# Optimization experiments

Measured on AMD Instinct MI355X. Metric: run time of the kernel, lower is better.

The kernel has to match this reference:

```python
import jax, jax.numpy as jnp
import numpy as np

N_NODES = 50000
N_EDGES = 500000
IN_FEATS = 96
OUT_FEATS = 128
N_ETYPES = 4
N_STEPS = 3  # feat is never updated (no GRU), so each step is identical


def setup_inputs() -> dict:
    key = jax.random.key(0)
    k1, k2, k3, k4, k5 = jax.random.split(key, 5)
    feat = jax.random.normal(k1, (N_NODES, IN_FEATS), dtype=jnp.float32)
    etypes = jax.random.randint(k2, (N_EDGES,), 0, N_ETYPES, dtype=jnp.int64)
    src = jax.random.randint(k3, (N_EDGES,), 0, N_NODES, dtype=jnp.int64)
    dst = jax.random.randint(k4, (N_EDGES,), 0, N_NODES, dtype=jnp.int64)
    # per-etype Linear(out_feats, out_feats): W[i] is [out, out], xavier-normal-ish
    gain = float(np.sqrt(2.0))  # calculate_gain('relu')
    std = gain * np.sqrt(2.0 / (OUT_FEATS + OUT_FEATS))
    W = jax.random.normal(k5, (N_ETYPES, OUT_FEATS, OUT_FEATS), dtype=jnp.float32) * std
    b = jnp.zeros((N_ETYPES, OUT_FEATS), dtype=jnp.float32)
    return {"feat": feat, "etypes": etypes, "src": src, "dst": dst, "W": W, "b": b}


def reference(feat, etypes, src, dst, W, b):
    n_nodes = feat.shape[0]
    # h_i^0 = [x_i || 0]  -> pad to out_feats
    h = jnp.pad(feat, ((0, 0), (0, OUT_FEATS - feat.shape[1])))  # [N, out]
    # Since there is no GRU, h never changes across n_steps; each step's 'a'
    # is identical, so one aggregation suffices (faithful to returned value).
    h_src = h[src]  # [E, out] gather
    msgs = jnp.zeros((h_src.shape[0], OUT_FEATS), dtype=h.dtype)
    for i in range(N_ETYPES):
        # Linear: x @ W_i^T + b_i, applied only to edges of type i
        m_i = h_src @ W[i].T + b[i]  # [E, out]
        msgs = jnp.where((etypes == i)[:, None], m_i, msgs)
    # scatter-sum messages to destination nodes
    a = jax.ops.segment_sum(msgs, dst, num_segments=n_nodes)  # [N, out]
    return a
```

## Files before the change

kernel.cpp:

```cpp
#include <hip/hip_runtime.h>
#include <hip/hip_bf16.h>

#define N_NODES 50000
#define N_EDGES 500000
#define IN_FEATS 96
#define OUT_FEATS 128
#define N_ETYPES 4
#define KCAT (N_ETYPES * IN_FEATS)

typedef __attribute__((ext_vector_type(8))) short short8;
typedef __attribute__((ext_vector_type(4))) float f32x4;

static __device__ inline short f2bf_bits(float f) {
    __hip_bfloat16 h = __float2bfloat16(f);
    return *reinterpret_cast<short*>(&h);
}
static __device__ inline unsigned pack2bf(float lo, float hi) {
    unsigned l = (unsigned short)f2bf_bits(lo);
    unsigned h = (unsigned short)f2bf_bits(hi);
    return l | (h << 16);
}

__global__ __launch_bounds__(256) void k_init(int* __restrict__ deg,
                                              const float* __restrict__ W,
                                              unsigned* __restrict__ Wb_u32) {
    int g = blockIdx.x * 256 + threadIdx.x;
    if (g < N_NODES) deg[g] = 0;
    if (g < 512 * 48) {
        int row = g / 48, pair = g % 48;
        float lo = W[(size_t)row * OUT_FEATS + pair * 2];
        float hi = W[(size_t)row * OUT_FEATS + pair * 2 + 1];
        Wb_u32[g] = pack2bf(lo, hi);
    }
}

__global__ __launch_bounds__(256) void k_hist(const int* __restrict__ dst,
                                              int* __restrict__ deg,
                                              int* __restrict__ rank) {
    int e = blockIdx.x * 256 + threadIdx.x;
    if (e < N_EDGES) rank[e] = atomicAdd(&deg[dst[e]], 1);
}

__global__ __launch_bounds__(256) void k_scan1(const int* __restrict__ in, int n,
                                               int* __restrict__ out, int* __restrict__ bsum) {
    int g = blockIdx.x * 256 + threadIdx.x;
    int lane = threadIdx.x & 63, wave = threadIdx.x >> 6;
    int v = (g < n) ? in[g] : 0;
    int orig = v;
    for (int off = 1; off < 64; off <<= 1) {
        int u = __shfl_up(v, off);
        if (lane >= off) v += u;
    }
    __shared__ int wsum[4];
    if (lane == 63) wsum[wave] = v;
    __syncthreads();
    if (threadIdx.x == 0) {
        int s = 0;
        for (int w = 0; w < 4; ++w) { int t = wsum[w]; wsum[w] = s; s += t; }
        bsum[blockIdx.x] = s;
    }
    __syncthreads();
    int excl = v - orig + wsum[wave];
    if (g < n) out[g] = excl;
}

__global__ __launch_bounds__(256) void k_scan3(int* __restrict__ pos, const int* __restrict__ bscan, int n) {
    int g = blockIdx.x * 256 + threadIdx.x;
    if (g < n) pos[g] += bscan[blockIdx.x];
}

__global__ __launch_bounds__(256) void k_bin(const int* __restrict__ dst, const int* __restrict__ src,
                                             const int* __restrict__ etypes,
                                             const int* __restrict__ pos, const int* __restrict__ rank,
                                             int* __restrict__ packed) {
    int e = blockIdx.x * 256 + threadIdx.x;
    if (e < N_EDGES) {
        int slot = pos[dst[e]] + rank[e];
        packed[slot] = src[e] | (etypes[e] << 16);
    }
}

__global__ __launch_bounds__(64) void k_agg(const float2* __restrict__ feat2,
                                            const int* __restrict__ pos, const int* __restrict__ deg,
                                            const int* __restrict__ packed,
                                            unsigned* __restrict__ Scat_u32,
                                            float* __restrict__ counts) {
    const int d = blockIdx.x;
    const int lane = threadIdx.x;
    const bool act = lane < 48;
    const int start = pos[d], cnt = deg[d];

    float2 a0 = {0.f, 0.f}, a1 = {0.f, 0.f}, a2 = {0.f, 0.f}, a3 = {0.f, 0.f};
    int c0 = 0, c1 = 0, c2 = 0, c3 = 0;
    const float2 zero = {0.f, 0.f};

    int i = 0;
    for (; i + 4 <= cnt; i += 4) {
        int p0 = packed[start + i + 0];
        int p1 = packed[start + i + 1];
        int p2 = packed[start + i + 2];
        int p3 = packed[start + i + 3];
        float2 v0 = act ? feat2[(size_t)(p0 & 0xFFFF) * 48 + lane] : zero;
        float2 v1 = act ? feat2[(size_t)(p1 & 0xFFFF) * 48 + lane] : zero;
        float2 v2 = act ? feat2[(size_t)(p2 & 0xFFFF) * 48 + lane] : zero;
        float2 v3 = act ? feat2[(size_t)(p3 & 0xFFFF) * 48 + lane] : zero;
        int e0 = p0 >> 16, e1 = p1 >> 16, e2 = p2 >> 16, e3 = p3 >> 16;
        if (e0 == 0) { a0.x += v0.x; a0.y += v0.y; ++c0; }
        else if (e0 == 1) { a1.x += v0.x; a1.y += v0.y; ++c1; }
        else if (e0 == 2) { a2.x += v0.x; a2.y += v0.y; ++c2; }
        else              { a3.x += v0.x; a3.y += v0.y; ++c3; }
        if (e1 == 0) { a0.x += v1.x; a0.y += v1.y; ++c0; }
        else if (e1 == 1) { a1.x += v1.x; a1.y += v1.y; ++c1; }
        else if (e1 == 2) { a2.x += v1.x; a2.y += v1.y; ++c2; }
        else              { a3.x += v1.x; a3.y += v1.y; ++c3; }
        if (e2 == 0) { a0.x += v2.x; a0.y += v2.y; ++c0; }
        else if (e2 == 1) { a1.x += v2.x; a1.y += v2.y; ++c1; }
        else if (e2 == 2) { a2.x += v2.x; a2.y += v2.y; ++c2; }
        else              { a3.x += v2.x; a3.y += v2.y; ++c3; }
        if (e3 == 0) { a0.x += v3.x; a0.y += v3.y; ++c0; }
        else if (e3 == 1) { a1.x += v3.x; a1.y += v3.y; ++c1; }
        else if (e3 == 2) { a2.x += v3.x; a2.y += v3.y; ++c2; }
        else              { a3.x += v3.x; a3.y += v3.y; ++c3; }
    }
    for (; i < cnt; ++i) {
        int p = packed[start + i];
        float2 v = act ? feat2[(size_t)(p & 0xFFFF) * 48 + lane] : zero;
        int e = p >> 16;
        if (e == 0) { a0.x += v.x; a0.y += v.y; ++c0; }
        else if (e == 1) { a1.x += v.x; a1.y += v.y; ++c1; }
        else if (e == 2) { a2.x += v.x; a2.y += v.y; ++c2; }
        else              { a3.x += v.x; a3.y += v.y; ++c3; }
    }

    if (act) {
        size_t base = (size_t)d * (KCAT / 2) + lane;
        Scat_u32[base]       = pack2bf(a0.x, a0.y);
        Scat_u32[base + 48]  = pack2bf(a1.x, a1.y);
        Scat_u32[base + 96]  = pack2bf(a2.x, a2.y);
        Scat_u32[base + 144] = pack2bf(a3.x, a3.y);
    }
    if (lane < 4) counts[d * 4 + lane] = (float)(lane == 0 ? c0 : lane == 1 ? c1 : lane == 2 ? c2 : c3);
}

#define LDT 104

__global__ __launch_bounds__(256) void k_gemm(const __hip_bfloat16* __restrict__ Scat,
                                              const short* __restrict__ Wb,
                                              const float* __restrict__ b,
                                              const float* __restrict__ counts,
                                              float* __restrict__ out) {
    __shared__ __align__(16) __hip_bfloat16 As[128][LDT];
    __shared__ __align__(16) __hip_bfloat16 Bs[128][LDT];
    const int m0 = blockIdx.x * 128;
    const int tid = threadIdx.x, lane = tid & 63, wave = tid >> 6;
    const int wm = wave >> 1, wn = wave & 1;

    f32x4 acc[4][4];
#pragma unroll
    for (int i = 0; i < 4; ++i)
#pragma unroll
        for (int jj = 0; jj < 4; ++jj) acc[i][jj] = (f32x4){0.f, 0.f, 0.f, 0.f};

    for (int ks = 0; ks < 4; ++ks) {
#pragma unroll
        for (int it = 0; it < 6; ++it) {
            int idx = tid + it * 256;
            int row = idx / 12, c8 = idx % 12;
            int gm = m0 + row;
            if (gm > N_NODES - 1) gm = N_NODES - 1;
            short8 v = *reinterpret_cast<const short8*>(&Scat[(size_t)gm * KCAT + ks * IN_FEATS + c8 * 8]);
            *reinterpret_cast<short8*>(&As[row][c8 * 8]) = v;
        }
#pragma unroll
        for (int it = 0; it < 6; ++it) {
            int idx = tid + it * 256;
            int row = idx / 12, c8 = idx % 12;
            short8 v = *reinterpret_cast<const short8*>(&Wb[((size_t)ks * OUT_FEATS + row) * IN_FEATS + c8 * 8]);
            *reinterpret_cast<short8*>(&Bs[row][c8 * 8]) = v;
        }
        __syncthreads();
#pragma unroll
        for (int kk = 0; kk < 3; ++kk) {
            short8 af[4], bf[4];
#pragma unroll
            for (int mi = 0; mi < 4; ++mi)
                af[mi] = *reinterpret_cast<const short8*>(&As[wm * 64 + mi * 16 + (lane & 15)][kk * 32 + (lane >> 4) * 8]);
#pragma unroll
            for (int ni = 0; ni < 4; ++ni)
                bf[ni] = *reinterpret_cast<const short8*>(&Bs[wn * 64 + ni * 16 + (lane & 15)][kk * 32 + (lane >> 4) * 8]);
#pragma unroll
            for (int mi = 0; mi < 4; ++mi)
#pragma unroll
                for (int ni = 0; ni < 4; ++ni)
                    acc[mi][ni] = __builtin_amdgcn_mfma_f32_16x16x32_bf16(af[mi], bf[ni], acc[mi][ni], 0, 0, 0);
        }
        __syncthreads();
    }

#pragma unroll
    for (int mi = 0; mi < 4; ++mi) {
#pragma unroll
        for (int r = 0; r < 4; ++r) {
            int m = m0 + wm * 64 + mi * 16 + (lane >> 4) * 4 + r;
            if (m < N_NODES) {
                float4 c4 = *reinterpret_cast<const float4*>(&counts[m * 4]);
#pragma unroll
                for (int ni = 0; ni < 4; ++ni) {
                    int n = wn * 64 + ni * 16 + (lane & 15);
                    float bias = c4.x * b[n] + c4.y * b[OUT_FEATS + n] +
                                 c4.z * b[2 * OUT_FEATS + n] + c4.w * b[3 * OUT_FEATS + n];
                    out[(size_t)m * OUT_FEATS + n] = acc[mi][ni][r] + bias;
                }
            }
        }
    }
}

__global__ __launch_bounds__(256) void edge_direct(const float* __restrict__ feat,
                                                   const int* __restrict__ etypes,
                                                   const int* __restrict__ src,
                                                   const int* __restrict__ dst,
                                                   const float* __restrict__ W,
                                                   const float* __restrict__ b,
                                                   float* __restrict__ out) {
    int gid = blockIdx.x * 256 + threadIdx.x;
    int e = gid >> 7;
    int j = gid & 127;
    if (e >= N_EDGES) return;
    int et = etypes[e];
    int s = src[e];
    int d = dst[e];
    const float* f = feat + (size_t)s * IN_FEATS;
    const float* w = W + ((size_t)et * OUT_FEATS + j) * OUT_FEATS;
    float acc = b[et * OUT_FEATS + j];
    for (int k = 0; k < IN_FEATS; ++k) acc += f[k] * w[k];
    atomicAdd(&out[(size_t)d * OUT_FEATS + j], acc);
}

extern "C" void kernel_launch(void* const* d_in, const int* in_sizes, int n_in,
                              void* d_out, int out_size, void* d_ws, size_t ws_size,
                              hipStream_t stream) {
    const float* feat  = (const float*)d_in[0];
    const int*   etyps = (const int*)d_in[1];
    const int*   src   = (const int*)d_in[2];
    const int*   dst   = (const int*)d_in[3];
    const float* W     = (const float*)d_in[4];
    const float* b     = (const float*)d_in[5];
    float* out = (float*)d_out;

    const size_t off_scat   = 0;
    const size_t off_counts = off_scat + (size_t)N_NODES * KCAT * 2;
    const size_t off_deg    = off_counts + (size_t)N_NODES * 4 * 4;
    const size_t off_pos    = off_deg + (size_t)N_NODES * 4;
    const size_t off_rank   = off_pos + (size_t)N_NODES * 4;
    const size_t off_packed = off_rank + (size_t)N_EDGES * 4;
    const size_t off_bsum   = off_packed + (size_t)N_EDGES * 4;
    const size_t off_bscan  = off_bsum + 1024;
    const size_t off_scrap  = off_bscan + 1024;
    const size_t off_wb     = off_scrap + 1024;
    const size_t need = off_wb + (size_t)512 * IN_FEATS * 2;

    if (ws_size >= need) {
        char* ws = (char*)d_ws;
        __hip_bfloat16* Scat = (__hip_bfloat16*)(ws + off_scat);
        unsigned* Scat_u32 = (unsigned*)(ws + off_scat);
        float* counts = (float*)(ws + off_counts);
        int* deg    = (int*)(ws + off_deg);
        int* pos    = (int*)(ws + off_pos);
        int* rank   = (int*)(ws + off_rank);
        int* packed = (int*)(ws + off_packed);
        int* bsum   = (int*)(ws + off_bsum);
        int* bscan  = (int*)(ws + off_bscan);
        int* scrap  = (int*)(ws + off_scrap);
        unsigned* Wb_u32 = (unsigned*)(ws + off_wb);
        short* Wb = (short*)(ws + off_wb);

        const int nScanBlocks = (N_NODES + 255) / 256;
        const int nEdgeBlocks = (N_EDGES + 255) / 256;

        k_init<<<nScanBlocks, 256, 0, stream>>>(deg, W, Wb_u32);
        k_hist<<<nEdgeBlocks, 256, 0, stream>>>(dst, deg, rank);
        k_scan1<<<nScanBlocks, 256, 0, stream>>>(deg, N_NODES, pos, bsum);
        k_scan1<<<1, 256, 0, stream>>>(bsum, nScanBlocks, bscan, scrap);
        k_scan3<<<nScanBlocks, 256, 0, stream>>>(pos, bscan, N_NODES);
        k_bin<<<nEdgeBlocks, 256, 0, stream>>>(dst, src, etyps, pos, rank, packed);
        k_agg<<<N_NODES, 64, 0, stream>>>((const float2*)feat, pos, deg, packed, Scat_u32, counts);
        k_gemm<<<(N_NODES + 127) / 128, 256, 0, stream>>>(Scat, Wb, b, counts, out);
    } else {
        hipMemsetAsync(d_out, 0, (size_t)out_size * sizeof(float), stream);
        int nthreads = N_EDGES * OUT_FEATS;
        edge_direct<<<nthreads / 256, 256, 0, stream>>>(feat, etyps, src, dst, W, b, out);
    }
}
```

Baseline: 100.2 us.

## Fuse block-sum scan into offset kernel and load GEMM operands directly

The separate single-block scan of block sums is removed. Each block of k_scan3 now reduces the preceding block sums itself (196 blocks, so one value per thread), which drops one kernel launch and the bscan/scrap buffers. Separately, k_gemm no longer stages A and B tiles through LDS with barriers. Each wave loads its MFMA fragments straight from global memory, trading LDS traffic and syncs for redundant global/L2 reads of A and W.

```diff
diff --git a/kernel.cpp b/kernel.cpp
--- a/kernel.cpp
+++ b/kernel.cpp
@@ -64,9 +64,21 @@
     if (g < n) out[g] = excl;
 }
 
-__global__ __launch_bounds__(256) void k_scan3(int* __restrict__ pos, const int* __restrict__ bscan, int n) {
-    int g = blockIdx.x * 256 + threadIdx.x;
-    if (g < n) pos[g] += bscan[blockIdx.x];
+__global__ __launch_bounds__(256) void k_scan3(int* __restrict__ pos, const int* __restrict__ bsum, int n) {
+    const int b = blockIdx.x;
+    const int t = threadIdx.x;
+    const int lane = t & 63, wave = t >> 6;
+    __shared__ int ws[4];
+    int v = (t < b) ? bsum[t] : 0;
+#pragma unroll
+    for (int off = 32; off > 0; off >>= 1) v += __shfl_down(v, off);
+    if (lane == 0) ws[wave] = v;
+    __syncthreads();
+    if (t == 0) ws[0] = ws[0] + ws[1] + ws[2] + ws[3];
+    __syncthreads();
+    int prefix = ws[0];
+    int g = b * 256 + t;
+    if (g < n) pos[g] += prefix;
 }
 
 __global__ __launch_bounds__(256) void k_bin(const int* __restrict__ dst, const int* __restrict__ src,
@@ -142,59 +154,55 @@
     if (lane < 4) counts[d * 4 + lane] = (float)(lane == 0 ? c0 : lane == 1 ? c1 : lane == 2 ? c2 : c3);
 }
 
-#define LDT 104
-
 __global__ __launch_bounds__(256) void k_gemm(const __hip_bfloat16* __restrict__ Scat,
                                               const short* __restrict__ Wb,
                                               const float* __restrict__ b,
                                               const float* __restrict__ counts,
                                               float* __restrict__ out) {
-    __shared__ __align__(16) __hip_bfloat16 As[128][LDT];
-    __shared__ __align__(16) __hip_bfloat16 Bs[128][LDT];
     const int m0 = blockIdx.x * 128;
     const int tid = threadIdx.x, lane = tid & 63, wave = tid >> 6;
     const int wm = wave >> 1, wn = wave & 1;
 
+    const __hip_bfloat16* abase[4];
+#pragma unroll
+    for (int mi = 0; mi < 4; ++mi) {
+        int row = m0 + wm * 64 + mi * 16 + (lane & 15);
+        if (row > N_NODES - 1) row = N_NODES - 1;
+        abase[mi] = Scat + (size_t)row * KCAT + (lane >> 4) * 8;
+    }
+    const short* bbase[4];
+#pragma unroll
+    for (int ni = 0; ni < 4; ++ni) {
+        int brow = wn * 64 + ni * 16 + (lane & 15);
+        bbase[ni] = Wb + (size_t)brow * IN_FEATS + (lane >> 4) * 8;
+    }
+
     f32x4 acc[4][4];
 #pragma unroll
     for (int i = 0; i < 4; ++i)
 #pragma unroll
         for (int jj = 0; jj < 4; ++jj) acc[i][jj] = (f32x4){0.f, 0.f, 0.f, 0.f};
 
+#pragma unroll
     for (int ks = 0; ks < 4; ++ks) {
-#pragma unroll
-        for (int it = 0; it < 6; ++it) {
-            int idx = tid + it * 256;
-            int row = idx / 12, c8 = idx % 12;
-            int gm = m0 + row;
-            if (gm > N_NODES - 1) gm = N_NODES - 1;
-            short8 v = *reinterpret_cast<const short8*>(&Scat[(size_t)gm * KCAT + ks * IN_FEATS + c8 * 8]);
-            *reinterpret_cast<short8*>(&As[row][c8 * 8]) = v;
+        short8 bf[3][4];
+#pragma unroll
+        for (int kk = 0; kk < 3; ++kk)
+#pragma unroll
+            for (int ni = 0; ni < 4; ++ni)
+                bf[kk][ni] = *reinterpret_cast<const short8*>(bbase[ni] + (size_t)ks * OUT_FEATS * IN_FEATS + kk * 32);
+#pragma unroll
+        for (int kk = 0; kk < 3; ++kk) {
+            short8 af[4];
+#pragma unroll
+            for (int mi = 0; mi < 4; ++mi)
+                af[mi] = *reinterpret_cast<const short8*>(abase[mi] + ks * IN_FEATS + kk * 32);
+#pragma unroll
+            for (int mi = 0; mi < 4; ++mi)
+#pragma unroll
+                for (int ni = 0; ni < 4; ++ni)
+                    acc[mi][ni] = __builtin_amdgcn_mfma_f32_16x16x32_bf16(af[mi], bf[kk][ni], acc[mi][ni], 0, 0, 0);
         }
-#pragma unroll
-        for (int it = 0; it < 6; ++it) {
-            int idx = tid + it * 256;
-            int row = idx / 12, c8 = idx % 12;
-            short8 v = *reinterpret_cast<const short8*>(&Wb[((size_t)ks * OUT_FEATS + row) * IN_FEATS + c8 * 8]);
-            *reinterpret_cast<short8*>(&Bs[row][c8 * 8]) = v;
-        }
-        __syncthreads();
-#pragma unroll
-        for (int kk = 0; kk < 3; ++kk) {
-            short8 af[4], bf[4];
-#pragma unroll
-            for (int mi = 0; mi < 4; ++mi)
-                af[mi] = *reinterpret_cast<const short8*>(&As[wm * 64 + mi * 16 + (lane & 15)][kk * 32 + (lane >> 4) * 8]);
-#pragma unroll
-            for (int ni = 0; ni < 4; ++ni)
-                bf[ni] = *reinterpret_cast<const short8*>(&Bs[wn * 64 + ni * 16 + (lane & 15)][kk * 32 + (lane >> 4) * 8]);
-#pragma unroll
-            for (int mi = 0; mi < 4; ++mi)
-#pragma unroll
-                for (int ni = 0; ni < 4; ++ni)
-                    acc[mi][ni] = __builtin_amdgcn_mfma_f32_16x16x32_bf16(af[mi], bf[ni], acc[mi][ni], 0, 0, 0);
-        }
-        __syncthreads();
     }
 
 #pragma unroll
@@ -255,9 +263,7 @@
     const size_t off_rank   = off_pos + (size_t)N_NODES * 4;
     const size_t off_packed = off_rank + (size_t)N_EDGES * 4;
     const size_t off_bsum   = off_packed + (size_t)N_EDGES * 4;
-    const size_t off_bscan  = off_bsum + 1024;
-    const size_t off_scrap  = off_bscan + 1024;
-    const size_t off_wb     = off_scrap + 1024;
+    const size_t off_wb     = off_bsum + 1024;
     const size_t need = off_wb + (size_t)512 * IN_FEATS * 2;
 
     if (ws_size >= need) {
@@ -270,8 +276,6 @@
         int* rank   = (int*)(ws + off_rank);
         int* packed = (int*)(ws + off_packed);
         int* bsum   = (int*)(ws + off_bsum);
-        int* bscan  = (int*)(ws + off_bscan);
-        int* scrap  = (int*)(ws + off_scrap);
         unsigned* Wb_u32 = (unsigned*)(ws + off_wb);
         short* Wb = (short*)(ws + off_wb);
 
@@ -281,8 +285,7 @@
         k_init<<<nScanBlocks, 256, 0, stream>>>(deg, W, Wb_u32);
         k_hist<<<nEdgeBlocks, 256, 0, stream>>>(dst, deg, rank);
         k_scan1<<<nScanBlocks, 256, 0, stream>>>(deg, N_NODES, pos, bsum);
-        k_scan1<<<1, 256, 0, stream>>>(bsum, nScanBlocks, bscan, scrap);
-        k_scan3<<<nScanBlocks, 256, 0, stream>>>(pos, bscan, N_NODES);
+        k_scan3<<<nScanBlocks, 256, 0, stream>>>(pos, bsum, N_NODES);
         k_bin<<<nEdgeBlocks, 256, 0, stream>>>(dst, src, etyps, pos, rank, packed);
         k_agg<<<N_NODES, 64, 0, stream>>>((const float2*)feat, pos, deg, packed, Scat_u32, counts);
         k_gemm<<<(N_NODES + 127) / 128, 256, 0, stream>>>(Scat, Wb, b, counts, out);
```

New measurement: 107.6 us. 1.07x slower.
